# Kernel tuning notes

Hardware: AMD Instinct MI355X
Metric: run time of the kernel (lower is better)

The kernel has to match this reference:

```python
import jax, jax.numpy as jnp
import numpy as np


def _agcn(x, node_embeddings, weights_pool, bias_pool, supports):
    # per-node weights: [N, dim_in, dim_out]
    weights = jnp.einsum('nd,dio->nio', node_embeddings, weights_pool)
    bias = node_embeddings @ bias_pool  # [N, dim_out]
    x_g = jnp.einsum('nm,bmc->bnc', supports, x)  # adaptive-adjacency aggregation
    return jnp.einsum('bni,nio->bno', x_g, weights) + bias


def setup_inputs() -> dict:
    key = jax.random.key(0)
    ks = jax.random.split(key, 7)
    B, N, D_IN, D_OUT, E = 64, 4096, 64, 64, 16
    return {
        'x': jax.random.normal(ks[0], (B, N, D_IN), dtype=jnp.float32),
        'state': jax.random.normal(ks[1], (B, N, D_OUT), dtype=jnp.float32),
        'node_embeddings': jax.random.normal(ks[2], (N, E), dtype=jnp.float32),
        'gate_weights_pool': jax.random.normal(ks[3], (E, D_IN + D_OUT, 2 * D_OUT), dtype=jnp.float32) * 0.1,
        'gate_bias_pool': jax.random.normal(ks[4], (E, 2 * D_OUT), dtype=jnp.float32) * 0.1,
        'update_weights_pool': jax.random.normal(ks[5], (E, D_IN + D_OUT, D_OUT), dtype=jnp.float32) * 0.1,
        'update_bias_pool': jax.random.normal(ks[6], (E, D_OUT), dtype=jnp.float32) * 0.1,
    }


def reference(x, state, node_embeddings, gate_weights_pool, gate_bias_pool,
              update_weights_pool, update_bias_pool) -> jnp.ndarray:
    hidden_dim = state.shape[-1]
    # learned adjacency shared by both GCNs: softmax(relu(E E^T), axis=1)
    supports = jax.nn.softmax(jax.nn.relu(node_embeddings @ node_embeddings.T), axis=1)
    input_and_state = jnp.concatenate([x, state], axis=-1)  # [B,N,dim_in+hidden]
    z_r = jax.nn.sigmoid(_agcn(input_and_state, node_embeddings,
                               gate_weights_pool, gate_bias_pool, supports))
    z, r = z_r[..., :hidden_dim], z_r[..., hidden_dim:]
    candidate = jnp.concatenate([x, z * state], axis=-1)
    hc = jnp.tanh(_agcn(candidate, node_embeddings,
                        update_weights_pool, update_bias_pool, supports))
    h = r * state + (1.0 - r) * hc
    return h
```

## Files before the change

### kernel.cpp

```cpp
#include <hip/hip_runtime.h>

typedef float f32x4 __attribute__((ext_vector_type(4)));
typedef float f32x16 __attribute__((ext_vector_type(16)));
typedef _Float16 f16x8 __attribute__((ext_vector_type(8)));
typedef _Float16 f16x4 __attribute__((ext_vector_type(4)));
typedef _Float16 f16x2 __attribute__((ext_vector_type(2)));

typedef __attribute__((address_space(1))) const unsigned char gbyte;
typedef __attribute__((address_space(3))) unsigned char sbyte;
__device__ __forceinline__ void gload_lds16(const void* gp, void* lp) {
  __builtin_amdgcn_global_load_lds((gbyte*)gp, (sbyte*)lp, 16, 0, 0);
}

__global__ __launch_bounds__(256) void k_wpoolT(const float* __restrict__ gwp,
                                                const float* __restrict__ uwp,
                                                float* __restrict__ wtg,
                                                float* __restrict__ wtu) {
  int idx = blockIdx.x * 256 + threadIdx.x;
  if (idx < 16 * 128 * 128) {
    int d = idx >> 14, rem = idx & 16383, o = rem >> 7, i = rem & 127;
    wtg[idx] = gwp[(d << 14) + (i << 7) + o];
  } else {
    int j = idx - 16 * 128 * 128;
    if (j < 16 * 64 * 128) {
      int d = j >> 13, rem = j & 8191, o = rem >> 7, i = rem & 127;
      wtu[j] = uwp[(d << 13) + (i << 6) + o];
    }
  }
}

__global__ __launch_bounds__(256) void k_supports(const float* __restrict__ emb,
                                                  _Float16* __restrict__ S) {
  int n0 = blockIdx.x * 4, tid = threadIdx.x;
  __shared__ float e_sh[4][16];
  __shared__ float red[4][4];
  if (tid < 16) {
    int r = tid >> 2, part = tid & 3;
    f32x4 v = *reinterpret_cast<const f32x4*>(emb + (n0 + r) * 16 + part * 4);
    *reinterpret_cast<f32x4*>(&e_sh[r][part * 4]) = v;
  }
  __syncthreads();
  float v[4][16];
  float sum[4] = {0.f, 0.f, 0.f, 0.f};
#pragma unroll
  for (int i = 0; i < 16; i++) {
    int m = i * 256 + tid;
    const f32x4* em = reinterpret_cast<const f32x4*>(emb + m * 16);
    f32x4 e0 = em[0], e1 = em[1], e2 = em[2], e3 = em[3];
#pragma unroll
    for (int r = 0; r < 4; r++) {
      float acc = 0.f;
#pragma unroll
      for (int q = 0; q < 4; q++) acc += e_sh[r][q] * e0[q];
#pragma unroll
      for (int q = 0; q < 4; q++) acc += e_sh[r][4 + q] * e1[q];
#pragma unroll
      for (int q = 0; q < 4; q++) acc += e_sh[r][8 + q] * e2[q];
#pragma unroll
      for (int q = 0; q < 4; q++) acc += e_sh[r][12 + q] * e3[q];
      acc = fmaxf(acc, 0.f);
      float e = __expf(acc);
      v[r][i] = e;
      sum[r] += e;
    }
  }
#pragma unroll
  for (int r = 0; r < 4; r++)
#pragma unroll
    for (int off = 32; off > 0; off >>= 1) sum[r] += __shfl_down(sum[r], off);
  if ((tid & 63) == 0) {
#pragma unroll
    for (int r = 0; r < 4; r++) red[tid >> 6][r] = sum[r];
  }
  __syncthreads();
  float inv[4];
#pragma unroll
  for (int r = 0; r < 4; r++)
    inv[r] = 1.f / (red[0][r] + red[1][r] + red[2][r] + red[3][r]);
#pragma unroll
  for (int i = 0; i < 16; i++)
#pragma unroll
    for (int r = 0; r < 4; r++)
      S[(size_t)(n0 + r) * 4096 + i * 256 + tid] = (_Float16)(v[r][i] * inv[r]);
}

__global__ __launch_bounds__(256) void k_concat(const float* __restrict__ x,
                                                const float* __restrict__ st,
                                                _Float16* __restrict__ xs_t) {
  int m0 = blockIdx.x * 64, b = blockIdx.y, tid = threadIdx.x;
  __shared__ __attribute__((aligned(16))) _Float16 T[64][130];
#pragma unroll
  for (int i = 0; i < 16; i++) {
    int li = i * 256 + tid;
    int ml = li >> 6, c = li & 63;
    int base = (b * 4096 + m0 + ml) * 64 + c;
    T[ml][c] = (_Float16)x[base];
    T[ml][64 + c] = (_Float16)st[base];
  }
  __syncthreads();
  int cg = tid >> 3, mch = tid & 7;
#pragma unroll
  for (int cb = 0; cb < 4; cb++) {
    int c = cb * 32 + cg;
    f16x8 tmp;
#pragma unroll
    for (int j = 0; j < 8; j++) tmp[j] = T[mch * 8 + j][c];
    *reinterpret_cast<f16x8*>(&xs_t[(b * 128 + c) * 4096 + m0 + mch * 8]) = tmp;
  }
}

__global__ __launch_bounds__(256) void k_gemm(const _Float16* __restrict__ S,
                                              const _Float16* __restrict__ Xt,
                                              _Float16* __restrict__ Y) {
  int nt = blockIdx.x & 31, b = blockIdx.x >> 5;
  int tid = threadIdx.x, lane = tid & 63, w = tid >> 6;
  int wr = w >> 1, wc = w & 1;
  __shared__ __attribute__((aligned(16))) _Float16 As[128 * 64];
  __shared__ __attribute__((aligned(16))) _Float16 Bs[128 * 64];
  const _Float16* Sb = S + nt * 128 * 4096;
  const _Float16* Xb = Xt + (size_t)b * 128 * 4096;
  f32x16 acc[2][2];
#pragma unroll
  for (int fm = 0; fm < 2; fm++)
#pragma unroll
    for (int fn = 0; fn < 2; fn++)
#pragma unroll
      for (int q = 0; q < 16; q++) acc[fm][fn][q] = 0.f;

  int lrow = lane >> 3;
  int lcolsw = (((lane & 7) ^ lrow) * 8);
  int r32 = lane & 31, hi32 = lane >> 5;
  int swz = (r32 & 7) * 8;
  for (int k0 = 0; k0 < 4096; k0 += 64) {
    __syncthreads();
#pragma unroll
    for (int i = 0; i < 4; i++) {
      int j = w * 4 + i;
      int row = j * 8 + lrow;
      gload_lds16(Sb + row * 4096 + k0 + lcolsw, &As[j * 512]);
      gload_lds16(Xb + row * 4096 + k0 + lcolsw, &Bs[j * 512]);
    }
    __syncthreads();
#pragma unroll
    for (int kk = 0; kk < 4; kk++) {
      int col = (kk * 16 + hi32 * 8) ^ swz;
      f16x8 af[2], bf[2];
#pragma unroll
      for (int fm = 0; fm < 2; fm++)
        af[fm] = *reinterpret_cast<const f16x8*>(&As[(wr * 64 + fm * 32 + r32) * 64 + col]);
#pragma unroll
      for (int fn = 0; fn < 2; fn++)
        bf[fn] = *reinterpret_cast<const f16x8*>(&Bs[(wc * 64 + fn * 32 + r32) * 64 + col]);
#pragma unroll
      for (int fm = 0; fm < 2; fm++)
#pragma unroll
        for (int fn = 0; fn < 2; fn++)
          acc[fm][fn] = __builtin_amdgcn_mfma_f32_32x32x16_f16(af[fm], bf[fn], acc[fm][fn], 0, 0, 0);
    }
  }
#pragma unroll
  for (int fm = 0; fm < 2; fm++)
#pragma unroll
    for (int fn = 0; fn < 2; fn++)
#pragma unroll
      for (int reg = 0; reg < 16; reg++) {
        int row = nt * 128 + wr * 64 + fm * 32 + (reg & 3) + 8 * (reg >> 2) + 4 * hi32;
        int c = wc * 64 + fn * 32 + r32;
        Y[((size_t)b * 4096 + row) * 128 + c] = (_Float16)acc[fm][fn][reg];
      }
}

__global__ __launch_bounds__(256) void k_gemm2(const _Float16* __restrict__ S,
                                               const _Float16* __restrict__ Xt,
                                               _Float16* __restrict__ Y) {
  int nt = blockIdx.x & 31, bp = blockIdx.x >> 5;
  int tid = threadIdx.x, lane = tid & 63, w = tid >> 6;
  int wr = w >> 1, wc = w & 1;
  __shared__ __attribute__((aligned(16))) _Float16 As[128 * 64];
  __shared__ __attribute__((aligned(16))) _Float16 Bs[128 * 64];
  const _Float16* Sb = S + nt * 128 * 4096;
  const _Float16* Xb = Xt + (size_t)(256 * bp + 64) * 4096;
  f32x16 acc[2][2];
#pragma unroll
  for (int fm = 0; fm < 2; fm++)
#pragma unroll
    for (int fn = 0; fn < 2; fn++)
#pragma unroll
      for (int q = 0; q < 16; q++) acc[fm][fn][q] = 0.f;

  int lrow = lane >> 3;
  int lcolsw = (((lane & 7) ^ lrow) * 8);
  int r32 = lane & 31, hi32 = lane >> 5;
  int swz = (r32 & 7) * 8;
  for (int k0 = 0; k0 < 4096; k0 += 64) {
    __syncthreads();
#pragma unroll
    for (int i = 0; i < 4; i++) {
      int j = w * 4 + i;
      int row = j * 8 + lrow;
      int groff = ((row >> 6) * 128 + (row & 63)) * 4096;
      gload_lds16(Sb + row * 4096 + k0 + lcolsw, &As[j * 512]);
      gload_lds16(Xb + groff + k0 + lcolsw, &Bs[j * 512]);
    }
    __syncthreads();
#pragma unroll
    for (int kk = 0; kk < 4; kk++) {
      int col = (kk * 16 + hi32 * 8) ^ swz;
      f16x8 af[2], bf[2];
#pragma unroll
      for (int fm = 0; fm < 2; fm++)
        af[fm] = *reinterpret_cast<const f16x8*>(&As[(wr * 64 + fm * 32 + r32) * 64 + col]);
#pragma unroll
      for (int fn = 0; fn < 2; fn++)
        bf[fn] = *reinterpret_cast<const f16x8*>(&Bs[(wc * 64 + fn * 32 + r32) * 64 + col]);
#pragma unroll
      for (int fm = 0; fm < 2; fm++)
#pragma unroll
        for (int fn = 0; fn < 2; fn++)
          acc[fm][fn] = __builtin_amdgcn_mfma_f32_32x32x16_f16(af[fm], bf[fn], acc[fm][fn], 0, 0, 0);
    }
  }
#pragma unroll
  for (int fm = 0; fm < 2; fm++)
#pragma unroll
    for (int fn = 0; fn < 2; fn++)
#pragma unroll
      for (int reg = 0; reg < 16; reg++) {
        int row = nt * 128 + wr * 64 + fm * 32 + (reg & 3) + 8 * (reg >> 2) + 4 * hi32;
        int ct = wc * 64 + fn * 32 + r32;
        int batch = 2 * bp + (ct >> 6);
        int c = 64 + (ct & 63);
        Y[((size_t)batch * 4096 + row) * 128 + c] = (_Float16)acc[fm][fn][reg];
      }
}

__global__ __launch_bounds__(256) void k_wall(const float* __restrict__ emb, int n0,
                                              const float* __restrict__ wt, int OI,
                                              _Float16* __restrict__ Wout) {
  int bx = blockIdx.x, by = blockIdx.y, tid = threadIdx.x;
  __shared__ float e_sh[64][16];
  {
    int node = tid >> 2, part = tid & 3;
    f32x4 v = *reinterpret_cast<const f32x4*>(emb + (n0 + bx * 64 + node) * 16 + part * 4);
    *reinterpret_cast<f32x4*>(&e_sh[node][part * 4]) = v;
  }
  __syncthreads();
  int oi0 = by * 2048 + tid * 8;
#pragma unroll
  for (int g = 0; g < 8; g++) {
    f32x4 a0[8], a1[8];
#pragma unroll
    for (int nn = 0; nn < 8; nn++) { a0[nn] = (f32x4){0,0,0,0}; a1[nn] = (f32x4){0,0,0,0}; }
#pragma unroll
    for (int d = 0; d < 16; d++) {
      const f32x4* p = reinterpret_cast<const f32x4*>(wt + d * OI + oi0);
      f32x4 v0 = p[0], v1 = p[1];
#pragma unroll
      for (int nn = 0; nn < 8; nn++) {
        float e = e_sh[g * 8 + nn][d];
        a0[nn] += e * v0;
        a1[nn] += e * v1;
      }
    }
#pragma unroll
    for (int nn = 0; nn < 8; nn++) {
      f16x8 pk;
#pragma unroll
      for (int q = 0; q < 4; q++) { pk[q] = (_Float16)a0[nn][q]; pk[4 + q] = (_Float16)a1[nn][q]; }
      int node = bx * 64 + g * 8 + nn;
      *reinterpret_cast<f16x8*>(Wout + (size_t)node * OI + oi0) = pk;
    }
  }
}

__global__ __launch_bounds__(256) void k_gate(const _Float16* __restrict__ xg,
                                              const float* __restrict__ emb,
                                              const _Float16* __restrict__ Wc,
                                              const float* __restrict__ gbp,
                                              int n0,
                                              _Float16* __restrict__ zb,
                                              _Float16* __restrict__ rb) {
  int n = n0 + blockIdx.x, tid = threadIdx.x, lane = tid & 63, w = tid >> 6;
  __shared__ __attribute__((aligned(16))) _Float16 As[64 * 64];
  __shared__ __attribute__((aligned(16))) _Float16 Bs[128 * 64];
  __shared__ float bias_sh[128];
  const _Float16* wrow = Wc + (size_t)blockIdx.x * 16384;
  if (tid < 128) {
    float s = 0.f;
#pragma unroll
    for (int d = 0; d < 16; d++) s += emb[n * 16 + d] * gbp[d * 128 + tid];
    bias_sh[tid] = s;
  }
  f32x16 acc[2];
#pragma unroll
  for (int fm = 0; fm < 2; fm++)
#pragma unroll
    for (int q = 0; q < 16; q++) acc[fm][q] = 0.f;

  int lrow = lane >> 3;
  int lcolsw = (((lane & 7) ^ lrow) * 8);
  int r32 = lane & 31, hi32 = lane >> 5;
  int swz = (r32 & 7) * 8;
  for (int k0 = 0; k0 < 128; k0 += 64) {
    __syncthreads();
#pragma unroll
    for (int i = 0; i < 2; i++) {
      int j = w * 2 + i;
      int row = j * 8 + lrow;
      gload_lds16(xg + ((size_t)row * 4096 + n) * 128 + k0 + lcolsw, &As[j * 512]);
    }
#pragma unroll
    for (int i = 0; i < 4; i++) {
      int j = w * 4 + i;
      int row = j * 8 + lrow;
      gload_lds16(wrow + row * 128 + k0 + lcolsw, &Bs[j * 512]);
    }
    __syncthreads();
#pragma unroll
    for (int kk = 0; kk < 4; kk++) {
      int col = (kk * 16 + hi32 * 8) ^ swz;
      f16x8 bf = *reinterpret_cast<const f16x8*>(&Bs[(w * 32 + r32) * 64 + col]);
#pragma unroll
      for (int fm = 0; fm < 2; fm++) {
        f16x8 af = *reinterpret_cast<const f16x8*>(&As[(fm * 32 + r32) * 64 + col]);
        acc[fm] = __builtin_amdgcn_mfma_f32_32x32x16_f16(af, bf, acc[fm], 0, 0, 0);
      }
    }
  }
  int o = w * 32 + r32;
  float bias = bias_sh[o];
#pragma unroll
  for (int fm = 0; fm < 2; fm++)
#pragma unroll
    for (int reg = 0; reg < 16; reg++) {
      int brow = fm * 32 + (reg & 3) + 8 * (reg >> 2) + 4 * hi32;
      float val = acc[fm][reg] + bias;
      float sg = 1.f / (1.f + __expf(-val));
      if (o < 64) zb[(n * 64 + brow) * 64 + o] = (_Float16)sg;
      else        rb[(n * 64 + brow) * 64 + (o - 64)] = (_Float16)sg;
    }
}

__global__ __launch_bounds__(256) void k_cand(const _Float16* __restrict__ zb,
                                              const float* __restrict__ st,
                                              _Float16* __restrict__ xs_t) {
  int m0 = blockIdx.x * 64, b = blockIdx.y, tid = threadIdx.x;
  __shared__ __attribute__((aligned(16))) _Float16 T[64][66];
#pragma unroll
  for (int i = 0; i < 16; i++) {
    int li = i * 256 + tid, ml = li >> 6, o = li & 63;
    float z = (float)zb[((m0 + ml) * 64 + b) * 64 + o];
    float s = st[(b * 4096 + m0 + ml) * 64 + o];
    T[ml][o] = (_Float16)(z * s);
  }
  __syncthreads();
  int og = tid >> 3, mch = tid & 7;
#pragma unroll
  for (int cb = 0; cb < 2; cb++) {
    int o = cb * 32 + og;
    f16x8 tmp;
#pragma unroll
    for (int j = 0; j < 8; j++) tmp[j] = T[mch * 8 + j][o];
    *reinterpret_cast<f16x8*>(&xs_t[(b * 128 + 64 + o) * 4096 + m0 + mch * 8]) = tmp;
  }
}

__global__ __launch_bounds__(256) void k_upd(const _Float16* __restrict__ xg2,
                                             const float* __restrict__ emb,
                                             const _Float16* __restrict__ Wc,
                                             const float* __restrict__ ubp,
                                             int n0,
                                             const _Float16* __restrict__ rb,
                                             const float* __restrict__ st,
                                             float* __restrict__ out) {
  int n = n0 + blockIdx.x, tid = threadIdx.x, lane = tid & 63, w = tid >> 6;
  int fm = w >> 1, fn = w & 1;
  __shared__ __attribute__((aligned(16))) _Float16 As[64 * 64];
  __shared__ __attribute__((aligned(16))) _Float16 Bs[64 * 64];
  __shared__ float bias_sh[64];
  const _Float16* wrow = Wc + (size_t)blockIdx.x * 8192;
  if (tid < 64) {
    float s = 0.f;
#pragma unroll
    for (int d = 0; d < 16; d++) s += emb[n * 16 + d] * ubp[d * 64 + tid];
    bias_sh[tid] = s;
  }
  f32x16 acc;
#pragma unroll
  for (int q = 0; q < 16; q++) acc[q] = 0.f;

  int lrow = lane >> 3;
  int lcolsw = (((lane & 7) ^ lrow) * 8);
  int r32 = lane & 31, hi32 = lane >> 5;
  int swz = (r32 & 7) * 8;
  for (int k0 = 0; k0 < 128; k0 += 64) {
    __syncthreads();
#pragma unroll
    for (int i = 0; i < 2; i++) {
      int j = w * 2 + i;
      int row = j * 8 + lrow;
      gload_lds16(xg2 + ((size_t)row * 4096 + n) * 128 + k0 + lcolsw, &As[j * 512]);
    }
#pragma unroll
    for (int i = 0; i < 2; i++) {
      int j = w * 2 + i;
      int row = j * 8 + lrow;
      gload_lds16(wrow + row * 128 + k0 + lcolsw, &Bs[j * 512]);
    }
    __syncthreads();
#pragma unroll
    for (int kk = 0; kk < 4; kk++) {
      int col = (kk * 16 + hi32 * 8) ^ swz;
      f16x8 af = *reinterpret_cast<const f16x8*>(&As[(fm * 32 + r32) * 64 + col]);
      f16x8 bf = *reinterpret_cast<const f16x8*>(&Bs[(fn * 32 + r32) * 64 + col]);
      acc = __builtin_amdgcn_mfma_f32_32x32x16_f16(af, bf, acc, 0, 0, 0);
    }
  }
  int o = fn * 32 + r32;
  float bias = bias_sh[o];
#pragma unroll
  for (int reg = 0; reg < 16; reg++) {
    int brow = fm * 32 + (reg & 3) + 8 * (reg >> 2) + 4 * hi32;
    float val = acc[reg] + bias;
    float e2 = __expf(2.f * val);
    float hc = 1.f - 2.f / (e2 + 1.f);
    float rr = (float)rb[(n * 64 + brow) * 64 + o];
    float s = st[((size_t)brow * 4096 + n) * 64 + o];
    out[((size_t)brow * 4096 + n) * 64 + o] = rr * s + (1.f - rr) * hc;
  }
}

extern "C" void kernel_launch(void* const* d_in, const int* in_sizes, int n_in,
                              void* d_out, int out_size, void* d_ws, size_t ws_size,
                              hipStream_t stream) {
  const float* x   = (const float*)d_in[0];
  const float* st  = (const float*)d_in[1];
  const float* emb = (const float*)d_in[2];
  const float* gwp = (const float*)d_in[3];
  const float* gbp = (const float*)d_in[4];
  const float* uwp = (const float*)d_in[5];
  const float* ubp = (const float*)d_in[6];
  float* out = (float*)d_out;
  char* ws = (char*)d_ws;

  _Float16* slotA = (_Float16*)(ws + 0);
  _Float16* xs_t  = (_Float16*)(ws + 33554432);
  _Float16* xg    = (_Float16*)(ws + 100663296);
  _Float16* zb    = (_Float16*)(ws + 167772160);
  _Float16* rb    = (_Float16*)(ws + 201326592);
  float* wtg = (float*)(ws + 234881024);
  float* wtu = (float*)(ws + 235929600);
  if (ws_size < 236453888ull) return;

  k_wpoolT<<<1536, 256, 0, stream>>>(gwp, uwp, wtg, wtu);
  k_supports<<<1024, 256, 0, stream>>>(emb, slotA);
  k_concat<<<dim3(64, 64), 256, 0, stream>>>(x, st, xs_t);
  k_gemm<<<2048, 256, 0, stream>>>(slotA, xs_t, xg);
  for (int c = 0; c < 2; c++) {
    k_wall<<<dim3(32, 8), 256, 0, stream>>>(emb, c * 2048, wtg, 16384, xs_t);
    k_gate<<<2048, 256, 0, stream>>>(xg, emb, xs_t, gbp, c * 2048, zb, rb);
  }
  k_cand<<<dim3(64, 64), 256, 0, stream>>>(zb, st, xs_t);
  k_gemm2<<<1024, 256, 0, stream>>>(slotA, xs_t, xg);
  for (int c = 0; c < 2; c++) {
    k_wall<<<dim3(32, 4), 256, 0, stream>>>(emb, c * 2048, wtu, 8192, zb);
    k_upd<<<2048, 256, 0, stream>>>(xg, emb, zb, ubp, c * 2048, rb, st, out);
  }
}
```

Measured before the change: 787.8 us.

## Enlarge GEMM block tile to 256 rows with 512-thread blocks

Both support-aggregation GEMMs now use 512-thread blocks that compute a 256x128 output tile instead of 128x128. Each staged X tile is reused across twice as many support rows, and the grid becomes 2D with half as many blocks. The intent is to cut global/L2 traffic for the X operand per FLOP. The cost is more LDS per block and fewer resident blocks, which may lower occupancy.

```diff
diff --git a/kernel.cpp b/kernel.cpp
--- a/kernel.cpp
+++ b/kernel.cpp
@@ -109,15 +109,15 @@
   }
 }
 
-__global__ __launch_bounds__(256) void k_gemm(const _Float16* __restrict__ S,
+__global__ __launch_bounds__(512) void k_gemm(const _Float16* __restrict__ S,
                                               const _Float16* __restrict__ Xt,
                                               _Float16* __restrict__ Y) {
-  int nt = blockIdx.x & 31, b = blockIdx.x >> 5;
+  int nt = blockIdx.x, b = blockIdx.y;
   int tid = threadIdx.x, lane = tid & 63, w = tid >> 6;
   int wr = w >> 1, wc = w & 1;
-  __shared__ __attribute__((aligned(16))) _Float16 As[128 * 64];
+  __shared__ __attribute__((aligned(16))) _Float16 As[256 * 64];
   __shared__ __attribute__((aligned(16))) _Float16 Bs[128 * 64];
-  const _Float16* Sb = S + nt * 128 * 4096;
+  const _Float16* Sb = S + (size_t)nt * 256 * 4096;
   const _Float16* Xb = Xt + (size_t)b * 128 * 4096;
   f32x16 acc[2][2];
 #pragma unroll
@@ -137,8 +137,13 @@
     for (int i = 0; i < 4; i++) {
       int j = w * 4 + i;
       int row = j * 8 + lrow;
-      gload_lds16(Sb + row * 4096 + k0 + lcolsw, &As[j * 512]);
-      gload_lds16(Xb + row * 4096 + k0 + lcolsw, &Bs[j * 512]);
+      gload_lds16(Sb + (size_t)row * 4096 + k0 + lcolsw, &As[j * 512]);
+    }
+#pragma unroll
+    for (int i = 0; i < 2; i++) {
+      int j = w * 2 + i;
+      int row = j * 8 + lrow;
+      gload_lds16(Xb + (size_t)row * 4096 + k0 + lcolsw, &Bs[j * 512]);
     }
     __syncthreads();
 #pragma unroll
@@ -164,21 +169,21 @@
     for (int fn = 0; fn < 2; fn++)
 #pragma unroll
       for (int reg = 0; reg < 16; reg++) {
-        int row = nt * 128 + wr * 64 + fm * 32 + (reg & 3) + 8 * (reg >> 2) + 4 * hi32;
+        int row = nt * 256 + wr * 64 + fm * 32 + (reg & 3) + 8 * (reg >> 2) + 4 * hi32;
         int c = wc * 64 + fn * 32 + r32;
         Y[((size_t)b * 4096 + row) * 128 + c] = (_Float16)acc[fm][fn][reg];
       }
 }
 
-__global__ __launch_bounds__(256) void k_gemm2(const _Float16* __restrict__ S,
+__global__ __launch_bounds__(512) void k_gemm2(const _Float16* __restrict__ S,
                                                const _Float16* __restrict__ Xt,
                                                _Float16* __restrict__ Y) {
-  int nt = blockIdx.x & 31, bp = blockIdx.x >> 5;
+  int nt = blockIdx.x, bp = blockIdx.y;
   int tid = threadIdx.x, lane = tid & 63, w = tid >> 6;
   int wr = w >> 1, wc = w & 1;
-  __shared__ __attribute__((aligned(16))) _Float16 As[128 * 64];
+  __shared__ __attribute__((aligned(16))) _Float16 As[256 * 64];
   __shared__ __attribute__((aligned(16))) _Float16 Bs[128 * 64];
-  const _Float16* Sb = S + nt * 128 * 4096;
+  const _Float16* Sb = S + (size_t)nt * 256 * 4096;
   const _Float16* Xb = Xt + (size_t)(256 * bp + 64) * 4096;
   f32x16 acc[2][2];
 #pragma unroll
@@ -198,9 +203,14 @@
     for (int i = 0; i < 4; i++) {
       int j = w * 4 + i;
       int row = j * 8 + lrow;
+      gload_lds16(Sb + (size_t)row * 4096 + k0 + lcolsw, &As[j * 512]);
+    }
+#pragma unroll
+    for (int i = 0; i < 2; i++) {
+      int j = w * 2 + i;
+      int row = j * 8 + lrow;
       int groff = ((row >> 6) * 128 + (row & 63)) * 4096;
-      gload_lds16(Sb + row * 4096 + k0 + lcolsw, &As[j * 512]);
-      gload_lds16(Xb + groff + k0 + lcolsw, &Bs[j * 512]);
+      gload_lds16(Xb + (size_t)groff + k0 + lcolsw, &Bs[j * 512]);
     }
     __syncthreads();
 #pragma unroll
@@ -226,7 +236,7 @@
     for (int fn = 0; fn < 2; fn++)
 #pragma unroll
       for (int reg = 0; reg < 16; reg++) {
-        int row = nt * 128 + wr * 64 + fm * 32 + (reg & 3) + 8 * (reg >> 2) + 4 * hi32;
+        int row = nt * 256 + wr * 64 + fm * 32 + (reg & 3) + 8 * (reg >> 2) + 4 * hi32;
         int ct = wc * 64 + fn * 32 + r32;
         int batch = 2 * bp + (ct >> 6);
         int c = 64 + (ct & 63);
@@ -455,13 +465,13 @@
   k_wpoolT<<<1536, 256, 0, stream>>>(gwp, uwp, wtg, wtu);
   k_supports<<<1024, 256, 0, stream>>>(emb, slotA);
   k_concat<<<dim3(64, 64), 256, 0, stream>>>(x, st, xs_t);
-  k_gemm<<<2048, 256, 0, stream>>>(slotA, xs_t, xg);
+  k_gemm<<<dim3(16, 64), 512, 0, stream>>>(slotA, xs_t, xg);
   for (int c = 0; c < 2; c++) {
     k_wall<<<dim3(32, 8), 256, 0, stream>>>(emb, c * 2048, wtg, 16384, xs_t);
     k_gate<<<2048, 256, 0, stream>>>(xg, emb, xs_t, gbp, c * 2048, zb, rb);
   }
   k_cand<<<dim3(64, 64), 256, 0, stream>>>(zb, st, xs_t);
-  k_gemm2<<<1024, 256, 0, stream>>>(slotA, xs_t, xg);
+  k_gemm2<<<dim3(16, 32), 512, 0, stream>>>(slotA, xs_t, xg);
   for (int c = 0; c < 2; c++) {
     k_wall<<<dim3(32, 4), 256, 0, stream>>>(emb, c * 2048, wtu, 8192, zb);
     k_upd<<<2048, 256, 0, stream>>>(xg, emb, zb, ubp, c * 2048, rb, st, out);
```

New measurement: 739.4 us. -6.1%, faster.
